# Kernel tuning notes

Measured on AMD Instinct MI355X. Metric: run time of the kernel, lower is better.

The kernel has to match this reference:

```python
import jax, jax.numpy as jnp
import numpy as np
from jax import lax

# config (matches init_kwargs)
HEADS = 4
KD2 = 256          # key_dim // 2
KNN = 16
BLOCK = 128        # knn * block_rate
COL = 512          # value_size // block
VALUE_SIZE = 65536 # key_num ** 2
D_OUT = 512
D_IN = 1024
QUERYDIM = HEADS * KD2  # 1024
KERNEL = 3


def setup_inputs() -> dict:
    key = jax.random.key(0)
    ks = jax.random.split(key, 8)
    B, T = 2, 2048
    return {
        "x": jax.random.normal(ks[0], (B, T, D_IN), dtype=jnp.float32),
        "conv_w": jax.random.normal(ks[1], (D_IN, 1, KERNEL), dtype=jnp.float32) * 0.1,
        "conv_b": jax.random.normal(ks[2], (D_IN,), dtype=jnp.float32) * 0.1,
        "lin_w": jax.random.normal(ks[3], (QUERYDIM, D_IN), dtype=jnp.float32) * (D_IN ** -0.5),
        "lin_b": jax.random.normal(ks[4], (QUERYDIM,), dtype=jnp.float32) * 0.1,
        "rowkeys": jax.random.normal(ks[5], (BLOCK, HEADS, KD2), dtype=jnp.float32) * (KD2 ** -0.5),
        "colkeys": jax.random.normal(ks[6], (COL, HEADS, KD2), dtype=jnp.float32) * (KD2 ** -0.5),
        "value_w": jax.random.normal(ks[7], (VALUE_SIZE, D_OUT), dtype=jnp.float32),
    }


def _forward(x, conv_w, conv_b, lin_w, lin_b, rowkeys, colkeys, value_w):
    B, T, C = x.shape
    # --- Querynet: causal depthwise conv1d + linear ---
    xt = jnp.transpose(x, (0, 2, 1))  # (B, C, T)
    y = lax.conv_general_dilated(
        xt, conv_w, window_strides=(1,), padding=[(KERNEL - 1, 0)],
        feature_group_count=C, dimension_numbers=("NCH", "OIH", "NCH"))
    y = y + conv_b[None, :, None]
    y = jnp.transpose(y, (0, 2, 1))                     # (B, T, C)
    query = y @ lin_w.T + lin_b                         # (B, T, querydim)
    # torch: query.view(B, heads, T, key_dim//2) -- raw C-order reshape
    q = query.reshape(B, HEADS, T, KD2)
    # --- block_wise_choice.get_indices ---
    score = jnp.einsum("bhtd,ehd->bhte", q, rowkeys)    # (B,H,T,block)
    col_scores = jnp.einsum("bhtd,chd->bhtc", q, colkeys)  # (B,H,T,col)
    score_col, idx_col = lax.top_k(col_scores, 1)       # (B,H,T,1)
    base = jnp.arange(BLOCK, dtype=jnp.int32)
    indices = base[None, None, None, :] * COL + idx_col  # (B,H,T,block)
    score = score + score_col                            # broadcast add
    # torch .view(B,H,-1,T): raw C-order reshape mixing tokens and blocks
    score = score.reshape(B, HEADS, BLOCK, T)
    indices = indices.reshape(B, HEADS, BLOCK, T)
    k = T * KNN // BLOCK
    score_top, dispatch = lax.top_k(score, k)            # (B,H,block,k), sorted desc
    idx_top = jnp.take_along_axis(indices, dispatch, axis=-1)
    score_r = score_top.reshape(B, BLOCK, -1)            # (B, block, H*k)
    idx_r = idx_top.reshape(B, BLOCK, -1)
    disp_r = dispatch.reshape(B, BLOCK, -1)
    # --- Memory_value: gather-weight-scatter ---
    gathered = value_w[idx_r]                            # (B, block, H*k, d)
    weighted = (gathered * score_r[..., None]).reshape(B, -1, D_OUT)
    flat_disp = disp_r.reshape(B, -1)                    # values in [0, T)
    out = jnp.zeros((B, T, D_OUT), dtype=weighted.dtype)
    out = out.at[jnp.arange(B)[:, None], flat_disp].add(weighted)
    return out


def reference(x, conv_w, conv_b, lin_w, lin_b, rowkeys, colkeys, value_w):
    return _forward(x, conv_w, conv_b, lin_w, lin_b, rowkeys, colkeys, value_w)
```

## Files before the change

### kernel.cpp

```cpp
#include <hip/hip_runtime.h>

constexpr int Bc   = 2;
constexpr int Tc   = 2048;
constexpr int Cc   = 1024;
constexpr int QDc  = 1024;
constexpr int Hc   = 4;
constexpr int KD2c = 256;
constexpr int BLKc = 128;
constexpr int COLc = 512;
constexpr int DOUTc= 512;
constexpr int KSELc= 256;
constexpr int NKEYS= BLKc + COLc;
constexpr int NBINS= Bc * Tc;
constexpr int NSEL = Bc * Hc * BLKc * KSELc;

typedef short bf16x8 __attribute__((ext_vector_type(8)));
typedef float f32x4  __attribute__((ext_vector_type(4)));

__device__ __forceinline__ unsigned short f2bf(float f) {
    unsigned u = __float_as_uint(f);
    u += 0x7FFFu + ((u >> 16) & 1u);
    return (unsigned short)(u >> 16);
}
__device__ __forceinline__ float bf2f(unsigned short h) {
    return __uint_as_float((unsigned)h << 16);
}
__device__ __forceinline__ void splitbf3(float f, unsigned short* h,
                                         unsigned short* m, unsigned short* l) {
    unsigned short hh = f2bf(f);
    float r1 = f - bf2f(hh);
    unsigned short mm = f2bf(r1);
    float r2 = r1 - bf2f(mm);
    *h = hh; *m = mm; *l = f2bf(r2);
}

__device__ __forceinline__ void gld_lds16(const void* g, void* l) {
    __builtin_amdgcn_global_load_lds(
        (const __attribute__((address_space(1))) unsigned int*)g,
        (__attribute__((address_space(3))) unsigned int*)l, 16, 0, 0);
}

__global__ __launch_bounds__(256) void conv_kernel(
    const float* __restrict__ x, const float* __restrict__ cw,
    const float* __restrict__ cb, unsigned short* __restrict__ y1,
    unsigned short* __restrict__ y2, unsigned short* __restrict__ y3)
{
    int idx = blockIdx.x * 256 + threadIdx.x;
    int c = idx & (Cc - 1);
    int t = (idx >> 10) & (Tc - 1);
    int b = idx >> 21;
    float w0 = cw[c*3+0], w1 = cw[c*3+1], w2 = cw[c*3+2];
    const float* xb = x + (size_t)b * Tc * Cc;
    float acc = cb[c] + w2 * xb[(size_t)t*Cc + c];
    if (t >= 1) acc += w1 * xb[(size_t)(t-1)*Cc + c];
    if (t >= 2) acc += w0 * xb[(size_t)(t-2)*Cc + c];
    splitbf3(acc, &y1[idx], &y2[idx], &y3[idx]);
}

__global__ __launch_bounds__(256) void convw_kernel(
    const float* __restrict__ w, unsigned short* __restrict__ w1,
    unsigned short* __restrict__ w2, unsigned short* __restrict__ w3)
{
    int idx = blockIdx.x * 256 + threadIdx.x;
    splitbf3(w[idx], &w1[idx], &w2[idx], &w3[idx]);
}

__global__ __launch_bounds__(256) void convkeys_kernel(
    const float* __restrict__ rowkeys, const float* __restrict__ colkeys,
    unsigned short* __restrict__ k1, unsigned short* __restrict__ k2,
    unsigned short* __restrict__ k3)
{
    int bid = blockIdx.x;
    int h = bid / NKEYS, n = bid % NKEYS;
    int k = threadIdx.x;
    float v = (n < BLKc) ? rowkeys[((size_t)n*Hc + h)*KD2c + k]
                         : colkeys[((size_t)(n-BLKc)*Hc + h)*KD2c + k];
    size_t o = ((size_t)h*NKEYS + n)*KD2c + k;
    splitbf3(v, &k1[o], &k2[o], &k3[o]);
}

__device__ __forceinline__ void mfma_gemm_tile(
    const unsigned short* __restrict__ A1g, const unsigned short* __restrict__ A2g,
    const unsigned short* __restrict__ A3g, int lda,
    const unsigned short* __restrict__ B1g, const unsigned short* __restrict__ B2g,
    const unsigned short* __restrict__ B3g, int ldb,
    int K, int m0, int n0, char* lds, f32x4 acc[4][2])
{
    const int tid  = threadIdx.x;
    const int wave = tid >> 6, lane = tid & 63;
    const int wr = wave >> 2, wc = wave & 3;
    const int g = lane >> 4, r16 = lane & 15;

    int aoff[4], boff[2];
    #pragma unroll
    for (int i = 0; i < 4; i++) {
        int ra = wr*64 + i*16 + r16;
        aoff[i] = ra*64 + ((g ^ ((ra>>1)&3)) << 4);
    }
    #pragma unroll
    for (int j = 0; j < 2; j++) {
        int rb = wc*32 + j*16 + r16;
        boff[j] = rb*64 + ((g ^ ((rb>>1)&3)) << 4);
    }
    const int row0 = tid >> 2, kg0 = ((tid & 3) ^ ((row0>>1)&3)) * 8;
    char* d0 = lds + wave*1024;

#define STAGE(kc, bo) do {                                                 \
        size_t a0_ = (size_t)(m0+row0)*lda + (kc) + kg0;                   \
        size_t b0_ = (size_t)(n0+row0)*ldb + (kc) + kg0;                   \
        gld_lds16(A1g + a0_, d0 + (bo));                                   \
        gld_lds16(A2g + a0_, d0 + 8192 + (bo));                            \
        gld_lds16(A3g + a0_, d0 + 16384 + (bo));                           \
        gld_lds16(B1g + b0_, d0 + 24576 + (bo));                           \
        gld_lds16(B2g + b0_, d0 + 32768 + (bo));                           \
        gld_lds16(B3g + b0_, d0 + 40960 + (bo));                           \
    } while (0)

    auto compute = [&](int bo) {
        bf16x8 a1[4], a2[4], a3[4], b1[2], b2[2], b3[2];
        #pragma unroll
        for (int i = 0; i < 4; i++) {
            a1[i] = *(const bf16x8*)(lds + bo + aoff[i]);
            a2[i] = *(const bf16x8*)(lds + bo +  8192 + aoff[i]);
            a3[i] = *(const bf16x8*)(lds + bo + 16384 + aoff[i]);
        }
        #pragma unroll
        for (int j = 0; j < 2; j++) {
            b1[j] = *(const bf16x8*)(lds + bo + 24576 + boff[j]);
            b2[j] = *(const bf16x8*)(lds + bo + 32768 + boff[j]);
            b3[j] = *(const bf16x8*)(lds + bo + 40960 + boff[j]);
        }
        #pragma unroll
        for (int i = 0; i < 4; i++)
            #pragma unroll
            for (int j = 0; j < 2; j++) {
                acc[i][j] = __builtin_amdgcn_mfma_f32_16x16x32_bf16(a3[i], b1[j], acc[i][j], 0, 0, 0);
                acc[i][j] = __builtin_amdgcn_mfma_f32_16x16x32_bf16(a2[i], b2[j], acc[i][j], 0, 0, 0);
                acc[i][j] = __builtin_amdgcn_mfma_f32_16x16x32_bf16(a1[i], b3[j], acc[i][j], 0, 0, 0);
                acc[i][j] = __builtin_amdgcn_mfma_f32_16x16x32_bf16(a2[i], b1[j], acc[i][j], 0, 0, 0);
                acc[i][j] = __builtin_amdgcn_mfma_f32_16x16x32_bf16(a1[i], b2[j], acc[i][j], 0, 0, 0);
                acc[i][j] = __builtin_amdgcn_mfma_f32_16x16x32_bf16(a1[i], b1[j], acc[i][j], 0, 0, 0);
            }
    };

    const int NT = K / 32;
    STAGE(0, 0);
    int bo = 0;
    for (int t = 0; t < NT - 1; ++t) {
        STAGE((t+1)*32, bo ^ 49152);
        asm volatile("s_waitcnt vmcnt(6)" ::: "memory");
        __builtin_amdgcn_s_barrier();
        asm volatile("" ::: "memory");
        compute(bo);
        asm volatile("" ::: "memory");
        __builtin_amdgcn_s_barrier();
        bo ^= 49152;
    }
    asm volatile("s_waitcnt vmcnt(0)" ::: "memory");
    __builtin_amdgcn_s_barrier();
    asm volatile("" ::: "memory");
    compute(bo);
#undef STAGE
}

__global__ __launch_bounds__(512) void qgemm_kernel(
    const unsigned short* __restrict__ y1, const unsigned short* __restrict__ y2,
    const unsigned short* __restrict__ y3,
    const unsigned short* __restrict__ w1, const unsigned short* __restrict__ w2,
    const unsigned short* __restrict__ w3,
    const float* __restrict__ bias,
    unsigned short* __restrict__ q1, unsigned short* __restrict__ q2,
    unsigned short* __restrict__ q3)
{
    __shared__ char lds[98304];
    int l = blockIdx.x;
    int yb = (l & 7) * 4 + ((l >> 3) & 3);
    int xb = l >> 5;
    int m0 = yb * 128, n0 = xb * 128;
    f32x4 acc[4][2];
    #pragma unroll
    for (int i = 0; i < 4; i++)
        #pragma unroll
        for (int j = 0; j < 2; j++) acc[i][j] = (f32x4)0.f;
    mfma_gemm_tile(y1, y2, y3, Cc, w1, w2, w3, Cc, Cc, m0, n0, lds, acc);

    const int lane = threadIdx.x & 63, wave = threadIdx.x >> 6;
    const int wr = wave >> 2, wc = wave & 3;
    const int g = lane >> 4, r16 = lane & 15;
    #pragma unroll
    for (int i = 0; i < 4; i++)
        #pragma unroll
        for (int j = 0; j < 2; j++)
            #pragma unroll
            for (int reg = 0; reg < 4; reg++) {
                int m = m0 + wr*64 + i*16 + g*4 + reg;
                int n = n0 + wc*32 + j*16 + r16;
                float v = acc[i][j][reg] + bias[n];
                size_t o = (size_t)m * QDc + n;
                splitbf3(v, &q1[o], &q2[o], &q3[o]);
            }
}

__global__ __launch_bounds__(512) void sgemm_kernel(
    const unsigned short* __restrict__ q1, const unsigned short* __restrict__ q2,
    const unsigned short* __restrict__ q3,
    const unsigned short* __restrict__ k1, const unsigned short* __restrict__ k2,
    const unsigned short* __restrict__ k3,
    float* __restrict__ Ctmp)
{
    __shared__ char lds[98304];
    int l = blockIdx.x;
    int b4h = l & 7;
    int m5  = l >> 3;
    int xb  = m5 % 5;
    int yb  = m5 / 5;
    size_t qo = (size_t)b4h * (Tc * KD2c);
    size_t ko = (size_t)(b4h & 3) * (NKEYS * KD2c);
    int m0 = yb * 128, n0 = xb * 128;
    f32x4 acc[4][2];
    #pragma unroll
    for (int i = 0; i < 4; i++)
        #pragma unroll
        for (int j = 0; j < 2; j++) acc[i][j] = (f32x4)0.f;
    mfma_gemm_tile(q1+qo, q2+qo, q3+qo, KD2c, k1+ko, k2+ko, k3+ko, KD2c,
                   KD2c, m0, n0, lds, acc);

    const int lane = threadIdx.x & 63, wave = threadIdx.x >> 6;
    const int wr = wave >> 2, wc = wave & 3;
    const int g = lane >> 4, r16 = lane & 15;
    float* Cb = Ctmp + (size_t)b4h * Tc * NKEYS;
    #pragma unroll
    for (int i = 0; i < 4; i++)
        #pragma unroll
        for (int j = 0; j < 2; j++)
            #pragma unroll
            for (int reg = 0; reg < 4; reg++) {
                int m = m0 + wr*64 + i*16 + g*4 + reg;
                int n = n0 + wc*32 + j*16 + r16;
                Cb[(size_t)m * NKEYS + n] = acc[i][j][reg];
            }
}

__global__ __launch_bounds__(256) void colmax_kernel(
    const float* __restrict__ Ctmp, float* __restrict__ s, int* __restrict__ cidx)
{
    int rid = blockIdx.x * 4 + (threadIdx.x >> 6);
    int lane = threadIdx.x & 63;
    const float* row = Ctmp + (size_t)rid * NKEYS;
    float best = -3.4e38f; int bi = 0;
    #pragma unroll
    for (int i = 0; i < 8; i++) {
        int c = lane + i*64;
        float v = row[BLKc + c];
        if (v > best) { best = v; bi = c; }
    }
    #pragma unroll
    for (int off = 32; off > 0; off >>= 1) {
        float ov = __shfl_xor(best, off, 64);
        int   oi = __shfl_xor(bi,   off, 64);
        if (ov > best || (ov == best && oi < bi)) { best = ov; bi = oi; }
    }
    if (lane == 0) cidx[rid] = bi;
    #pragma unroll
    for (int e = lane; e < BLKc; e += 64)
        s[(size_t)rid*BLKc + e] = row[e] + best;
}

__global__ __launch_bounds__(256) void topk_kernel(
    const float* __restrict__ s, const int* __restrict__ cidx,
    int* __restrict__ tk_j, int* __restrict__ tk_vidx, float* __restrict__ tk_score)
{
    int wid  = (blockIdx.x << 2) + (threadIdx.x >> 6);
    int lane = threadIdx.x & 63;
    int batch = wid >> 7;
    int i = wid & 127;
    const float* srow = s + (size_t)batch * (Tc*BLKc) + (size_t)i * 2048;

    unsigned key[8][4];
    #pragma unroll
    for (int r = 0; r < 8; r++) {
        float4 v4 = *(const float4*)&srow[r*256 + lane*4];
        float vv[4] = {v4.x, v4.y, v4.z, v4.w};
        #pragma unroll
        for (int e = 0; e < 4; e++) {
            unsigned u = __float_as_uint(vv[e]);
            key[r][e] = (u >> 31) ? ~u : (u | 0x80000000u);
        }
    }

    unsigned lo = 0, hi = 0xFFFFFFFFu;
    while (lo < hi) {
        unsigned d = hi - lo;
        unsigned mid = lo + ((d >> 1) + (d & 1u));
        int cnt = 0;
        #pragma unroll
        for (int r = 0; r < 8; r++)
            #pragma unroll
            for (int e = 0; e < 4; e++)
                cnt += (key[r][e] >= mid) ? 1 : 0;
        #pragma unroll
        for (int off = 32; off > 0; off >>= 1) cnt += __shfl_xor(cnt, off, 64);
        if (cnt >= KSELc) lo = mid; else hi = mid - 1;
    }
    const unsigned thr = lo;

    int gcnt = 0, ecnt = 0;
    unsigned eqmask = 0;
    #pragma unroll
    for (int r = 0; r < 8; r++)
        #pragma unroll
        for (int e = 0; e < 4; e++) {
            gcnt += (key[r][e] > thr) ? 1 : 0;
            if (key[r][e] == thr) { eqmask |= (1u << (r*4+e)); ecnt++; }
        }

    int gpre = gcnt, epre = ecnt;
    #pragma unroll
    for (int off = 1; off < 64; off <<= 1) {
        int gv = __shfl_up(gpre, off, 64);
        int ev = __shfl_up(epre, off, 64);
        if (lane >= off) { gpre += gv; epre += ev; }
    }
    const int total_greater = __shfl(gpre, 63, 64);
    const int total_eq      = __shfl(epre, 63, 64);
    const int gbase = gpre - gcnt;
    const int ebase = epre - ecnt;
    const int need  = KSELc - total_greater;

    const size_t obase = (size_t)wid * KSELc;
    const int cbase = batch * Tc + i * 16;

    int rk = 0;
    #pragma unroll
    for (int r = 0; r < 8; r++)
        #pragma unroll
        for (int e = 0; e < 4; e++) {
            if (key[r][e] > thr) {
                int j = r*256 + lane*4 + e;
                unsigned u = key[r][e];
                float f = (u >> 31) ? __uint_as_float(u ^ 0x80000000u)
                                    : __uint_as_float(~u);
                size_t o = obase + gbase + rk;
                tk_j[o] = j;
                tk_vidx[o] = (j & 127) * COLc + cidx[cbase + (j >> 7)];
                tk_score[o] = f;
                rk++;
            }
        }

    if (need == total_eq) {
        int erk = 0;
        #pragma unroll
        for (int r = 0; r < 8; r++)
            #pragma unroll
            for (int e = 0; e < 4; e++) {
                if (key[r][e] == thr) {
                    int j = r*256 + lane*4 + e;
                    float f = (thr >> 31) ? __uint_as_float(thr ^ 0x80000000u)
                                          : __uint_as_float(~thr);
                    size_t o = obase + total_greater + ebase + erk;
                    tk_j[o] = j;
                    tk_vidx[o] = (j & 127) * COLc + cidx[cbase + (j >> 7)];
                    tk_score[o] = f;
                    erk++;
                }
            }
    } else {
        unsigned em = eqmask;
        int left = need;
        while (left > 0) {
            int myj = 0x7FFFFFFF;
            if (em) {
                int bit = __builtin_ctz(em);
                myj = (bit >> 2)*256 + lane*4 + (bit & 3);
            }
            int mn = myj;
            #pragma unroll
            for (int off = 32; off > 0; off >>= 1) mn = min(mn, __shfl_xor(mn, off, 64));
            if (myj == mn) {
                em &= em - 1;
                int j = mn;
                float f = (thr >> 31) ? __uint_as_float(thr ^ 0x80000000u)
                                      : __uint_as_float(~thr);
                size_t o = obase + (KSELc - left);
                tk_j[o] = j;
                tk_vidx[o] = (j & 127) * COLc + cidx[cbase + (j >> 7)];
                tk_score[o] = f;
            }
            left--;
        }
    }
}

__global__ __launch_bounds__(256) void zero_bins_kernel(int* __restrict__ p, int n)
{
    int i = blockIdx.x * 256 + threadIdx.x;
    if (i < n) p[i] = 0;
}

__global__ __launch_bounds__(256) void count_kernel(
    const int* __restrict__ tk_j, int* __restrict__ counts)
{
    int idx = blockIdx.x * 256 + threadIdx.x;
    int r = idx >> 8;
    int b = r >> 9;
    int j = tk_j[idx];
    atomicAdd(&counts[b * Tc + j], 1);
}

__global__ __launch_bounds__(256) void scan_kernel(
    const int* __restrict__ counts, int* __restrict__ offsets)
{
    __shared__ int part[256];
    int tid = threadIdx.x;
    int local[16];
    int sum = 0;
    #pragma unroll
    for (int k = 0; k < 16; k++) { local[k] = sum; sum += counts[tid*16 + k]; }
    part[tid] = sum;
    __syncthreads();
    for (int st = 1; st < 256; st <<= 1) {
        int v = (tid >= st) ? part[tid - st] : 0;
        __syncthreads();
        part[tid] += v;
        __syncthreads();
    }
    int base = (tid == 0) ? 0 : part[tid - 1];
    #pragma unroll
    for (int k = 0; k < 16; k++) offsets[tid*16 + k] = base + local[k];
    if (tid == 255) offsets[NBINS] = base + sum;
}

__global__ __launch_bounds__(256) void fill_kernel(
    const int* __restrict__ tk_j, const int* __restrict__ tk_vidx,
    const float* __restrict__ tk_score, const int* __restrict__ offsets,
    int* __restrict__ fillctr, int* __restrict__ bin_vidx,
    float* __restrict__ bin_score)
{
    int idx = blockIdx.x * 256 + threadIdx.x;
    int r = idx >> 8;
    int b = r >> 9;
    int bin = b * Tc + tk_j[idx];
    int pos = offsets[bin] + atomicAdd(&fillctr[bin], 1);
    bin_vidx[pos]  = tk_vidx[idx];
    bin_score[pos] = tk_score[idx];
}

__global__ __launch_bounds__(256) void gather_kernel(
    const int* __restrict__ offsets, const int* __restrict__ bin_vidx,
    const float* __restrict__ bin_score, const float* __restrict__ value_w,
    float* __restrict__ out)
{
    __shared__ int   svidx[512];
    __shared__ float sscore[512];
    int x = blockIdx.x;
    int xcd  = x & 7;
    int rank = x >> 3;
    int sl   = rank >> 5;
    int wbin = rank & 31;
    int e    = sl * 8 + xcd;
    int b    = wbin >> 4;
    int jj   = wbin & 15;
    int bin  = b * Tc + jj * 128 + e;

    int tid = threadIdx.x;
    int beg = offsets[bin], cnt = offsets[bin + 1] - beg;
    for (int n = tid; n < cnt; n += 256) {
        svidx[n]  = bin_vidx[beg + n];
        sscore[n] = bin_score[beg + n];
    }
    __syncthreads();

    const int c = tid * 2;
    float accx = 0.f, accy = 0.f;
    int n = 0;
    for (; n + 8 <= cnt; n += 8) {
        int vi[8]; float sc[8]; float2 vv[8];
        #pragma unroll
        for (int k = 0; k < 8; k++) { vi[k] = svidx[n+k]; sc[k] = sscore[n+k]; }
        #pragma unroll
        for (int k = 0; k < 8; k++)
            vv[k] = *(const float2*)&value_w[(size_t)vi[k] * DOUTc + c];
        #pragma unroll
        for (int k = 0; k < 8; k++) { accx += sc[k]*vv[k].x; accy += sc[k]*vv[k].y; }
    }
    for (; n < cnt; n++) {
        int v = svidx[n]; float sc = sscore[n];
        float2 a = *(const float2*)&value_w[(size_t)v * DOUTc + c];
        accx += sc*a.x; accy += sc*a.y;
    }
    float2 res; res.x = accx; res.y = accy;
    *(float2*)&out[(size_t)bin * DOUTc + c] = res;
}

extern "C" void kernel_launch(void* const* d_in, const int* in_sizes, int n_in,
                              void* d_out, int out_size, void* d_ws, size_t ws_size,
                              hipStream_t stream)
{
    const float* x       = (const float*)d_in[0];
    const float* conv_w  = (const float*)d_in[1];
    const float* conv_b  = (const float*)d_in[2];
    const float* lin_w   = (const float*)d_in[3];
    const float* lin_b   = (const float*)d_in[4];
    const float* rowkeys = (const float*)d_in[5];
    const float* colkeys = (const float*)d_in[6];
    const float* value_w = (const float*)d_in[7];
    float* out = (float*)d_out;

    constexpr size_t MB = 1024*1024;
    char* w = (char*)d_ws;
    float*          Ctmp = (float*)(w);
    unsigned short* y1   = (unsigned short*)(w);
    unsigned short* y2   = (unsigned short*)(w +  8*MB);
    unsigned short* y3   = (unsigned short*)(w + 16*MB);
    unsigned short* w1   = (unsigned short*)(w + 24*MB);
    unsigned short* w2   = (unsigned short*)(w + 26*MB);
    unsigned short* w3   = (unsigned short*)(w + 28*MB);
    unsigned short* q1   = (unsigned short*)(w + 40*MB);
    unsigned short* q2   = (unsigned short*)(w + 48*MB);
    unsigned short* q3   = (unsigned short*)(w + 56*MB);
    unsigned short* k1   = (unsigned short*)(w + 64*MB);
    unsigned short* k2   = (unsigned short*)(w + 66*MB);
    unsigned short* k3   = (unsigned short*)(w + 68*MB);
    float*          s    = (float*)(w + 70*MB);
    int*            cidx = (int*)  (w + 78*MB);
    int*            tk_j = (int*)  (w + 79*MB);
    int*            tk_v = (int*)  (w + 80*MB);
    float*          tk_s = (float*)(w + 81*MB);
    int*            counts    = (int*)  (w + 82*MB);
    int*            offsets   = (int*)  (w + 82*MB + 32768);
    int*            fillctr   = (int*)  (w + 82*MB + 65536);
    int*            bin_vidx  = (int*)  (w + 82*MB + 131072);
    float*          bin_score = (float*)(w + 82*MB + 131072 + 1048576);

    conv_kernel<<<(Bc*Tc*Cc)/256, 256, 0, stream>>>(x, conv_w, conv_b, y1, y2, y3);
    convw_kernel<<<(QDc*Cc)/256, 256, 0, stream>>>(lin_w, w1, w2, w3);
    convkeys_kernel<<<Hc*NKEYS, 256, 0, stream>>>(rowkeys, colkeys, k1, k2, k3);
    qgemm_kernel<<<256, 512, 0, stream>>>(
        y1, y2, y3, w1, w2, w3, lin_b, q1, q2, q3);
    sgemm_kernel<<<640, 512, 0, stream>>>(
        q1, q2, q3, k1, k2, k3, Ctmp);
    colmax_kernel<<<(Bc*Hc*Tc)/4, 256, 0, stream>>>(Ctmp, s, cidx);
    topk_kernel<<<Bc*Hc*BLKc/4, 256, 0, stream>>>(s, cidx, tk_j, tk_v, tk_s);
    zero_bins_kernel<<<(96*1024/4 + 255)/256, 256, 0, stream>>>(counts, 96*1024/4);
    count_kernel<<<NSEL/256, 256, 0, stream>>>(tk_j, counts);
    scan_kernel<<<1, 256, 0, stream>>>(counts, offsets);
    fill_kernel<<<NSEL/256, 256, 0, stream>>>(tk_j, tk_v, tk_s, offsets,
                                              fillctr, bin_vidx, bin_score);
    gather_kernel<<<NBINS, 256, 0, stream>>>(offsets, bin_vidx, bin_score,
                                             value_w, out);
}
```

Baseline: 223.6 us.

## Fuse bin counting into top-k and split gather across two thread halves

Bin counts are now computed with atomics inside the top-k kernel, which removes the separate count kernel and its reread of tk_j. The zero-bins kernel moves to the start of the launch sequence. The gather kernel now runs 512 threads per bin: each half accumulates alternate entries and the two partial sums are combined through shared memory, which exposes more memory-level parallelism for the value-row loads. The cost is extra atomics inside top-k and an added barrier plus reduction in gather.

```diff
diff --git a/kernel.cpp b/kernel.cpp
--- a/kernel.cpp
+++ b/kernel.cpp
@@ -268,13 +268,15 @@
 
 __global__ __launch_bounds__(256) void topk_kernel(
     const float* __restrict__ s, const int* __restrict__ cidx,
-    int* __restrict__ tk_j, int* __restrict__ tk_vidx, float* __restrict__ tk_score)
+    int* __restrict__ tk_j, int* __restrict__ tk_vidx, float* __restrict__ tk_score,
+    int* __restrict__ counts)
 {
     int wid  = (blockIdx.x << 2) + (threadIdx.x >> 6);
     int lane = threadIdx.x & 63;
     int batch = wid >> 7;
     int i = wid & 127;
     const float* srow = s + (size_t)batch * (Tc*BLKc) + (size_t)i * 2048;
+    int* bcounts = counts + (wid >> 9) * Tc;
 
     unsigned key[8][4];
     #pragma unroll
@@ -344,6 +346,7 @@
                 tk_j[o] = j;
                 tk_vidx[o] = (j & 127) * COLc + cidx[cbase + (j >> 7)];
                 tk_score[o] = f;
+                atomicAdd(&bcounts[j], 1);
                 rk++;
             }
         }
@@ -362,6 +365,7 @@
                     tk_j[o] = j;
                     tk_vidx[o] = (j & 127) * COLc + cidx[cbase + (j >> 7)];
                     tk_score[o] = f;
+                    atomicAdd(&bcounts[j], 1);
                     erk++;
                 }
             }
@@ -386,6 +390,7 @@
                 tk_j[o] = j;
                 tk_vidx[o] = (j & 127) * COLc + cidx[cbase + (j >> 7)];
                 tk_score[o] = f;
+                atomicAdd(&bcounts[j], 1);
             }
             left--;
         }
@@ -396,16 +401,6 @@
 {
     int i = blockIdx.x * 256 + threadIdx.x;
     if (i < n) p[i] = 0;
-}
-
-__global__ __launch_bounds__(256) void count_kernel(
-    const int* __restrict__ tk_j, int* __restrict__ counts)
-{
-    int idx = blockIdx.x * 256 + threadIdx.x;
-    int r = idx >> 8;
-    int b = r >> 9;
-    int j = tk_j[idx];
-    atomicAdd(&counts[b * Tc + j], 1);
 }
 
 __global__ __launch_bounds__(256) void scan_kernel(
@@ -446,13 +441,14 @@
     bin_score[pos] = tk_score[idx];
 }
 
-__global__ __launch_bounds__(256) void gather_kernel(
+__global__ __launch_bounds__(512) void gather_kernel(
     const int* __restrict__ offsets, const int* __restrict__ bin_vidx,
     const float* __restrict__ bin_score, const float* __restrict__ value_w,
     float* __restrict__ out)
 {
     __shared__ int   svidx[512];
     __shared__ float sscore[512];
+    __shared__ float px[256], py[256];
     int x = blockIdx.x;
     int xcd  = x & 7;
     int rank = x >> 3;
@@ -463,34 +459,41 @@
     int jj   = wbin & 15;
     int bin  = b * Tc + jj * 128 + e;
 
-    int tid = threadIdx.x;
+    int tid  = threadIdx.x;
+    int half = tid >> 8;
+    int ct   = tid & 255;
     int beg = offsets[bin], cnt = offsets[bin + 1] - beg;
-    for (int n = tid; n < cnt; n += 256) {
+    for (int n = tid; n < cnt; n += 512) {
         svidx[n]  = bin_vidx[beg + n];
         sscore[n] = bin_score[beg + n];
     }
     __syncthreads();
 
-    const int c = tid * 2;
+    const int c = ct * 2;
     float accx = 0.f, accy = 0.f;
-    int n = 0;
-    for (; n + 8 <= cnt; n += 8) {
+    int n = half;
+    for (; n + 14 < cnt; n += 16) {
         int vi[8]; float sc[8]; float2 vv[8];
         #pragma unroll
-        for (int k = 0; k < 8; k++) { vi[k] = svidx[n+k]; sc[k] = sscore[n+k]; }
+        for (int k = 0; k < 8; k++) { vi[k] = svidx[n+2*k]; sc[k] = sscore[n+2*k]; }
         #pragma unroll
         for (int k = 0; k < 8; k++)
             vv[k] = *(const float2*)&value_w[(size_t)vi[k] * DOUTc + c];
         #pragma unroll
         for (int k = 0; k < 8; k++) { accx += sc[k]*vv[k].x; accy += sc[k]*vv[k].y; }
     }
-    for (; n < cnt; n++) {
+    for (; n < cnt; n += 2) {
         int v = svidx[n]; float sc = sscore[n];
         float2 a = *(const float2*)&value_w[(size_t)v * DOUTc + c];
         accx += sc*a.x; accy += sc*a.y;
     }
-    float2 res; res.x = accx; res.y = accy;
-    *(float2*)&out[(size_t)bin * DOUTc + c] = res;
+    if (half) { px[ct] = accx; py[ct] = accy; }
+    __syncthreads();
+    if (!half) {
+        accx += px[ct]; accy += py[ct];
+        float2 res; res.x = accx; res.y = accy;
+        *(float2*)&out[(size_t)bin * DOUTc + c] = res;
+    }
 }
 
 extern "C" void kernel_launch(void* const* d_in, const int* in_sizes, int n_in,
@@ -533,6 +536,7 @@
     int*            bin_vidx  = (int*)  (w + 82*MB + 131072);
     float*          bin_score = (float*)(w + 82*MB + 131072 + 1048576);
 
+    zero_bins_kernel<<<(96*1024/4 + 255)/256, 256, 0, stream>>>(counts, 96*1024/4);
     conv_kernel<<<(Bc*Tc*Cc)/256, 256, 0, stream>>>(x, conv_w, conv_b, y1, y2, y3);
     convw_kernel<<<(QDc*Cc)/256, 256, 0, stream>>>(lin_w, w1, w2, w3);
     convkeys_kernel<<<Hc*NKEYS, 256, 0, stream>>>(rowkeys, colkeys, k1, k2, k3);
@@ -541,12 +545,10 @@
     sgemm_kernel<<<640, 512, 0, stream>>>(
         q1, q2, q3, k1, k2, k3, Ctmp);
     colmax_kernel<<<(Bc*Hc*Tc)/4, 256, 0, stream>>>(Ctmp, s, cidx);
-    topk_kernel<<<Bc*Hc*BLKc/4, 256, 0, stream>>>(s, cidx, tk_j, tk_v, tk_s);
-    zero_bins_kernel<<<(96*1024/4 + 255)/256, 256, 0, stream>>>(counts, 96*1024/4);
-    count_kernel<<<NSEL/256, 256, 0, stream>>>(tk_j, counts);
+    topk_kernel<<<Bc*Hc*BLKc/4, 256, 0, stream>>>(s, cidx, tk_j, tk_v, tk_s, counts);
     scan_kernel<<<1, 256, 0, stream>>>(counts, offsets);
     fill_kernel<<<NSEL/256, 256, 0, stream>>>(tk_j, tk_v, tk_s, offsets,
                                               fillctr, bin_vidx, bin_score);
-    gather_kernel<<<NBINS, 256, 0, stream>>>(offsets, bin_vidx, bin_score,
+    gather_kernel<<<NBINS, 512, 0, stream>>>(offsets, bin_vidx, bin_score,
                                              value_w, out);
 }
```

After: 249.2 us. 11.5% more time.
